# Optimization experiments

Hardware: AMD Instinct MI355X
Metric: run time of the kernel (lower is better)

Reference implementation:

```python
import jax, jax.numpy as jnp
import numpy as np
import math

B, N, E, H = 2, 2048, 1024, 16
D = E // H

def setup_inputs() -> dict:
    key = jax.random.key(0)
    ks = jax.random.split(key, 9)
    s = 1.0 / math.sqrt(E)
    return {
        "x": jax.random.normal(ks[0], (B, N, E), dtype=jnp.float32),
        "Wq": jax.random.uniform(ks[1], (E, E), jnp.float32, -s, s),
        "bq": jax.random.uniform(ks[2], (E,), jnp.float32, -s, s),
        "Wk": jax.random.uniform(ks[3], (E, E), jnp.float32, -s, s),
        "bk": jax.random.uniform(ks[4], (E,), jnp.float32, -s, s),
        "Wv": jax.random.uniform(ks[5], (E, E), jnp.float32, -s, s),
        "bv": jax.random.uniform(ks[6], (E,), jnp.float32, -s, s),
        "Wo": jax.random.uniform(ks[7], (E, E), jnp.float32, -s, s),
        "bo": jax.random.uniform(ks[8], (E,), jnp.float32, -s, s),
    }

def _split_heads(t):
    # [b, n, (h d)] -> [b, h, n, d]
    b, n, _ = t.shape
    return t.reshape(b, n, H, D).transpose(0, 2, 1, 3)

def reference(x, Wq, bq, Wk, bk, Wv, bv, Wo, bo):
    q = _split_heads(x @ Wq.T + bq)
    k = _split_heads(x @ Wk.T + bk)
    v = _split_heads(x @ Wv.T + bv)
    energy = jnp.einsum('bhqd,bhkd->bhqk', q, k)
    # Faithful to source: softmax first, THEN divide by sqrt(n_embedding)
    attention = jax.nn.softmax(energy, axis=-1) / jnp.sqrt(jnp.float32(E))
    out = jnp.einsum('bhqk,bhkd->bhqd', attention, v)
    out = out.transpose(0, 2, 1, 3).reshape(x.shape[0], x.shape[1], E)
    return out @ Wo.T + bo
```

## Files before the change

kernel.cpp:

```cpp
#include <hip/hip_runtime.h>


typedef __bf16 bf16x8 __attribute__((ext_vector_type(8)));
typedef float  f32x4  __attribute__((ext_vector_type(4)));
typedef float  f32x16 __attribute__((ext_vector_type(16)));
using u16 = unsigned short;
using u32 = unsigned int;
typedef u16 u16x8 __attribute__((ext_vector_type(8)));
typedef u16 u16x4 __attribute__((ext_vector_type(4)));
typedef u32 u32x4 __attribute__((ext_vector_type(4)));

constexpr int BATCH = 2, SEQ = 2048, EMB = 1024, NH = 16, HD = 64;
constexpr int MTOT = BATCH * SEQ;
constexpr int KTOT = EMB;
constexpr int NTOT = EMB;
constexpr float LOG2E = 1.44269504088896340736f;

constexpr size_t OFF_XBF = 0;
constexpr size_t OFF_WQ  = 8u * 1024 * 1024;
constexpr size_t OFF_WK  = OFF_WQ + 2u * 1024 * 1024;
constexpr size_t OFF_WV  = OFF_WK + 2u * 1024 * 1024;
constexpr size_t OFF_WO  = OFF_WV + 2u * 1024 * 1024;
constexpr size_t OFF_Q   = OFF_WO + 2u * 1024 * 1024;
constexpr size_t OFF_K   = OFF_Q  + 8u * 1024 * 1024;
constexpr size_t OFF_VT  = OFF_K  + 8u * 1024 * 1024;

__device__ __forceinline__ u16 f2bf(float f) {
  u32 u = __builtin_bit_cast(u32, f);
  u = (u + 0x7fffu + ((u >> 16) & 1u)) >> 16;
  return (u16)u;
}

__device__ __forceinline__ bf16x8 ld_bf16x8(const u16* p) {
  return __builtin_bit_cast(bf16x8, *(const u16x8*)p);
}

__device__ __forceinline__ float fexp2(float x) {
#if __has_builtin(__builtin_amdgcn_exp2f)
  return __builtin_amdgcn_exp2f(x);
#else
  return exp2f(x);
#endif
}

__device__ __forceinline__ float fmax3(float a, float b, float c) {
  float d;
  asm("v_max3_f32 %0, %1, %2, %3" : "=v"(d) : "v"(a), "v"(b), "v"(c));
  return d;
}

__device__ __forceinline__ u32 cvtpk(float lo, float hi_) {
  u32 r;
  asm("v_cvt_pk_bf16_f32 %0, %1, %2" : "=v"(r) : "v"(lo), "v"(hi_));
  return r;
}

__device__ __forceinline__ void stage16(const void* g, void* l) {
#if __has_builtin(__builtin_amdgcn_global_load_lds)
  __builtin_amdgcn_global_load_lds(
      (__attribute__((address_space(1))) void*)const_cast<void*>(g),
      (__attribute__((address_space(3))) void*)l, 16, 0, 0);
#else
  int lane = threadIdx.x & 63;
  uint4 v = *(const uint4*)g;
  *(uint4*)((char*)l + lane * 16) = v;
#endif
}

__global__ __launch_bounds__(256) void cvt_all(
    const float* __restrict__ x, const float* __restrict__ wq,
    const float* __restrict__ wk, const float* __restrict__ wv,
    const float* __restrict__ wo, u16* __restrict__ ox, u16* __restrict__ oq,
    u16* __restrict__ okk, u16* __restrict__ ov, u16* __restrict__ oo) {
  int id = blockIdx.x;
  const float* in;
  u16* out;
  int i;
  if (id < 4096) {
    in = x; out = ox; i = id * 256 + threadIdx.x;
  } else {
    int z = (id - 4096) >> 10, r = (id - 4096) & 1023;
    in = (z == 0) ? wq : (z == 1) ? wk : (z == 2) ? wv : wo;
    out = (z == 0) ? oq : (z == 1) ? okk : (z == 2) ? ov : oo;
    i = r * 256 + threadIdx.x;
  }
  float4 f = ((const float4*)in)[i];
  u32 lo = (u32)f2bf(f.x) | ((u32)f2bf(f.y) << 16);
  u32 hi = (u32)f2bf(f.z) | ((u32)f2bf(f.w) << 16);
  ((uint2*)out)[i] = make_uint2(lo, hi);
}

__device__ __forceinline__ void gemm_bt_core(const u16* __restrict__ A,
                                             const u16* __restrict__ Bm,
                                             const float* __restrict__ bias,
                                             void* __restrict__ out, int mode,
                                             float oscale) {
  __shared__ __align__(16) u16 smem[2][128 * 32];
  u16* sA = smem[0];
  u16* sB = smem[1];
  const int tid = threadIdx.x, w = tid >> 6, ln = tid & 63;
  const int wr = w >> 1, wc = w & 1, qq = ln >> 4, t = ln & 15;
  const int m0 = blockIdx.y * 128, n0 = blockIdx.x * 128;

  f32x4 acc[4][4] = {};

  for (int kt = 0; kt < KTOT; kt += 32) {
#pragma unroll
    for (int j = 0; j < 2; j++) {
      int ck = w * 128 + j * 64 + ln;
      int r = ck >> 2, c2 = ck & 3;
      stage16(&A[(size_t)(m0 + r) * KTOT + kt + c2 * 8], &sA[(w * 128 + j * 64) * 8]);
      stage16(&Bm[(size_t)(n0 + r) * KTOT + kt + c2 * 8], &sB[(w * 128 + j * 64) * 8]);
    }
    __syncthreads();

    bf16x8 av[4], bv[4];
#pragma unroll
    for (int f = 0; f < 4; f++) {
      av[f] = ld_bf16x8(&sA[(wr * 64 + f * 16 + t) * 32 + qq * 8]);
      bv[f] = ld_bf16x8(&sB[(wc * 64 + f * 16 + t) * 32 + qq * 8]);
    }
#pragma unroll
    for (int i = 0; i < 4; i++)
#pragma unroll
      for (int j = 0; j < 4; j++)
        acc[i][j] = __builtin_amdgcn_mfma_f32_16x16x32_bf16(av[i], bv[j], acc[i][j], 0, 0, 0);
    __syncthreads();
  }

  if (mode == 1) {
    u16* tb = (u16*)smem;
    const int b = m0 >> 11, tokb = (m0 & 2047) + t * 8;
#pragma unroll
    for (int ph = 0; ph < 2; ph++) {
      if (ph == 1) __syncthreads();
      if (wc == ph) {
#pragma unroll
        for (int fc = 0; fc < 4; fc++) {
          int nl = fc * 16 + t;
          float bn = bias[n0 + ph * 64 + nl];
#pragma unroll
          for (int fr = 0; fr < 4; fr++)
#pragma unroll
            for (int i = 0; i < 4; i++) {
              int ml = wr * 64 + fr * 16 + qq * 4 + i;
              tb[nl * 128 + (ml ^ ((nl & 7) << 4))] = f2bf(acc[fr][fc][i] + bn);
            }
        }
      }
      __syncthreads();
#pragma unroll
      for (int s = 0; s < 4; s++) {
        int row = w * 16 + s * 4 + qq;
        int n = n0 + ph * 64 + row;
        int hh = n >> 6, d = n & 63;
        u16x8 vd = *(const u16x8*)&tb[row * 128 + ((t * 8) ^ ((row & 7) << 4))];
        *(u16x8*)&((u16*)out)[(((size_t)(b * NH + hh)) * HD + d) * SEQ + tokb] = vd;
      }
    }
    return;
  }

#pragma unroll
  for (int fc = 0; fc < 4; fc++) {
    int n = n0 + wc * 64 + fc * 16 + t;
    float bn = bias[n];
#pragma unroll
    for (int fr = 0; fr < 4; fr++) {
#pragma unroll
      for (int i = 0; i < 4; i++) {
        int m = m0 + wr * 64 + fr * 16 + qq * 4 + i;
        float v = (acc[fr][fc][i] + bn) * oscale;
        if (mode == 2) {
          ((float*)out)[(size_t)m * NTOT + n] = v;
        } else {
          int b = m >> 11, tok = m & 2047, h = n >> 6, d = n & 63;
          ((u16*)out)[(((size_t)(b * NH + h)) * SEQ + tok) * HD + d] = f2bf(v);
        }
      }
    }
  }
}

__global__ __launch_bounds__(256) void gemm_qkv(
    const u16* __restrict__ A, const u16* __restrict__ WQ, const u16* __restrict__ WK,
    const u16* __restrict__ WV, const float* __restrict__ bq, const float* __restrict__ bk,
    const float* __restrict__ bv, u16* Qo, u16* Ko, u16* Vo) {
  int z = blockIdx.z;
  const u16* Bm = (z == 0) ? WQ : ((z == 1) ? WK : WV);
  const float* bias = (z == 0) ? bq : ((z == 1) ? bk : bv);
  u16* out = (z == 0) ? Qo : ((z == 1) ? Ko : Vo);
  gemm_bt_core(A, Bm, bias, out, (z == 2) ? 1 : 0, (z == 0) ? LOG2E : 1.0f);
}

__global__ __launch_bounds__(256) void gemm_o(const u16* __restrict__ A,
                                              const u16* __restrict__ WO,
                                              const float* __restrict__ bo,
                                              float* __restrict__ out) {
  gemm_bt_core(A, WO, bo, out, 2, 1.0f);
}

__global__ __launch_bounds__(512, 4) void flash_attn(const u16* __restrict__ Q,
                                                     const u16* __restrict__ Kg,
                                                     const u16* __restrict__ VT,
                                                     u16* __restrict__ O) {
  const int e = blockIdx.x;
  const int xcd = e & 7, slot = e >> 3;
  const int bh = xcd * 4 + (slot & 3);
  const int qt = slot >> 2;

  const int tid = threadIdx.x, w = tid >> 6, ln = tid & 63;
  const int c = ln & 31, hi = ln >> 5;
  const int kb = w >> 2;
  const int q0 = qt * 128 + (w & 3) * 32;

  const u16* Qb = Q + (size_t)bh * SEQ * HD;
  const u16* Kb = Kg + (size_t)bh * SEQ * HD;
  const u16* Vb = VT + (size_t)bh * HD * SEQ;

  __shared__ __align__(16) u16 sK[2][64 * 64];
  __shared__ __align__(16) u16 sV[2][64 * 64];
  __shared__ float2 sml[8][64];

  bf16x8 qf[4];
#pragma unroll
  for (int ks = 0; ks < 4; ks++)
    qf[ks] = ld_bf16x8(&Qb[(size_t)(q0 + c) * HD + ks * 16 + hi * 8]);

  const bf16x8 ones = __builtin_bit_cast(
      bf16x8, (u16x8){0x3f80, 0x3f80, 0x3f80, 0x3f80, 0x3f80, 0x3f80, 0x3f80, 0x3f80});

  f32x16 ot[2];
  ot[0] = 0.f; ot[1] = 0.f;
  f32x16 acc_l = 0.f;
  float m = -1e30f;

#define STAGE(buf, kt)                                                         \
  {                                                                            \
    int ck = w * 64 + ln;                                                      \
    int r = ck >> 3, c2 = ck & 7, c2s = c2 ^ (r & 7);                          \
    stage16(&Kb[(size_t)((kt) + r) * HD + c2s * 8],                            \
            &sK[buf][(size_t)(w * 64) * 8]);                                   \
    stage16(&Vb[(size_t)r * SEQ + (kt) + c2s * 8],                             \
            &sV[buf][(size_t)(w * 64) * 8]);                                   \
  }

  STAGE(0, 0)
  __syncthreads();

  int it = 0;
  for (int kt = 0; kt < SEQ; kt += 64, it ^= 1) {
    if (kt + 64 < SEQ) STAGE(it ^ 1, kt + 64)
    const u16* kbuf = sK[it];
    const u16* vbuf = sV[it];

    f32x16 st = 0.f;
    __builtin_amdgcn_s_setprio(1);
#pragma unroll
    for (int ks = 0; ks < 4; ks++) {
      int row = kb * 32 + c;
      int boff = ((2 * ks + hi) ^ (row & 7)) << 4;
      bf16x8 kf = ld_bf16x8((const u16*)((const char*)(kbuf + row * 64) + boff));
      st = __builtin_amdgcn_mfma_f32_32x32x16_bf16(kf, qf[ks], st, 0, 0, 0);
    }
    __builtin_amdgcn_s_setprio(0);

    float a0 = fmax3(st[0], st[1], st[2]);
    float a1 = fmax3(st[3], st[4], st[5]);
    float a2 = fmax3(st[6], st[7], st[8]);
    float a3 = fmax3(st[9], st[10], st[11]);
    float a4 = fmax3(st[12], st[13], st[14]);
    float a5 = fmaxf(st[15], a0);
    float b0 = fmax3(a1, a2, a3);
    float b1 = fmax3(a4, a5, b0);
    float pmax = fmaxf(b1, __shfl_xor(b1, 32));

    if (!__all(pmax <= m + 8.0f)) {
      float mn = fmaxf(m, pmax);
      float sc = fexp2(m - mn);
      acc_l[0] *= sc;
#pragma unroll
      for (int i = 0; i < 16; i++) { ot[0][i] *= sc; ot[1][i] *= sc; }
      m = mn;
    }

#pragma unroll
    for (int i = 0; i < 16; i++) st[i] = fexp2(st[i] - m);

    bf16x8 pb[2];
#pragma unroll
    for (int ks2 = 0; ks2 < 2; ks2++) {
      const int R0 = 8 * ks2;
      const int R1 = 4 * ((2 * ks2 + 1) & 3);
      u32 X0 = cvtpk(st[R0], st[R0 + 1]);
      u32 X1 = cvtpk(st[R0 + 2], st[R0 + 3]);
      u32 Y0 = cvtpk(st[R1], st[R1 + 1]);
      u32 Y1 = cvtpk(st[R1 + 2], st[R1 + 3]);
      asm("v_permlane32_swap_b32 %0, %1" : "+v"(X0), "+v"(Y0));
      asm("v_permlane32_swap_b32 %0, %1" : "+v"(X1), "+v"(Y1));
      u32x4 wd; wd.x = X0; wd.y = X1; wd.z = Y0; wd.w = Y1;
      pb[ks2] = __builtin_bit_cast(bf16x8, wd);
    }

    __builtin_amdgcn_s_setprio(1);
#pragma unroll
    for (int ks2 = 0; ks2 < 2; ks2++) {
#pragma unroll
      for (int db = 0; db < 2; db++) {
        int row = db * 32 + c;
        int boff = ((kb * 4 + ks2 * 2 + hi) ^ (row & 7)) << 4;
        bf16x8 vf = ld_bf16x8((const u16*)((const char*)(vbuf + row * 64) + boff));
        ot[db] = __builtin_amdgcn_mfma_f32_32x32x16_bf16(vf, pb[ks2], ot[db], 0, 0, 0);
      }
      acc_l = __builtin_amdgcn_mfma_f32_32x32x16_bf16(ones, pb[ks2], acc_l, 0, 0, 0);
    }
    __builtin_amdgcn_s_setprio(0);
    __syncthreads();
  }
#undef STAGE

  float myl = acc_l[0];
  const int pair = w & 3;
  float* xA = (float*)sK;
  float* xB = (float*)sV;
  {
    f32x16 give = (w < 4) ? ot[1] : ot[0];
    *(f32x16*)((w < 4 ? xA : xB) + (size_t)(pair * 64 + ln) * 16) = give;
    sml[w][ln] = make_float2(m, myl);
  }
  __syncthreads();

  float2 po = sml[w ^ 4][ln];
  float M2 = fmaxf(m, po.x);
  float s_me = fexp2(m - M2), s_po = fexp2(po.x - M2);
  float lf = myl * s_me + po.y * s_po;
  float inv = 1.0f / (lf * 32.0f);
  f32x16 oth = *(const f32x16*)((w < 4 ? xB : xA) + (size_t)(pair * 64 + ln) * 16);
  f32x16 own = (w < 4) ? ot[0] : ot[1];
  const int db = (w < 4) ? 0 : 1;

  const int b = bh >> 4, h = bh & 15;
  u16* obase = O + ((size_t)(b * SEQ + q0 + c)) * EMB + h * HD;
#pragma unroll
  for (int g = 0; g < 4; g++) {
    u16x4 pkt;
#pragma unroll
    for (int i = 0; i < 4; i++)
      pkt[i] = f2bf((own[g * 4 + i] * s_me + oth[g * 4 + i] * s_po) * inv);
    *(u16x4*)(obase + db * 32 + g * 8 + hi * 4) = pkt;
  }
}

extern "C" void kernel_launch(void* const* d_in, const int* in_sizes, int n_in,
                              void* d_out, int out_size, void* d_ws, size_t ws_size,
                              hipStream_t stream) {
  const float* x  = (const float*)d_in[0];
  const float* Wq = (const float*)d_in[1];
  const float* bq = (const float*)d_in[2];
  const float* Wk = (const float*)d_in[3];
  const float* bk = (const float*)d_in[4];
  const float* Wv = (const float*)d_in[5];
  const float* bv = (const float*)d_in[6];
  const float* Wo = (const float*)d_in[7];
  const float* bo = (const float*)d_in[8];

  char* ws = (char*)d_ws;
  u16* xbf = (u16*)(ws + OFF_XBF);
  u16* wqb = (u16*)(ws + OFF_WQ);
  u16* wkb = (u16*)(ws + OFF_WK);
  u16* wvb = (u16*)(ws + OFF_WV);
  u16* wob = (u16*)(ws + OFF_WO);
  u16* Qw  = (u16*)(ws + OFF_Q);
  u16* Kw  = (u16*)(ws + OFF_K);
  u16* Vw  = (u16*)(ws + OFF_VT);

  cvt_all<<<dim3(8192), 256, 0, stream>>>(x, Wq, Wk, Wv, Wo, xbf, wqb, wkb, wvb, wob);

  gemm_qkv<<<dim3(NTOT / 128, MTOT / 128, 3), 256, 0, stream>>>(
      xbf, wqb, wkb, wvb, bq, bk, bv, Qw, Kw, Vw);

  flash_attn<<<dim3(512), 512, 0, stream>>>(Qw, Kw, Vw, xbf);

  gemm_o<<<dim3(NTOT / 128, MTOT / 128), 256, 0, stream>>>(xbf, wob, bo, (float*)d_out);
}
```

Measured before the change: 136.0 us.

## Double-buffer GEMM staging and software-pipeline QK^T ahead of softmax in attention

The projection GEMM core now double-buffers its A/B shared-memory tiles, so the next K-slice loads while the current one is multiplied, leaving one barrier per iteration instead of two. The flash attention kernel moves to triple-buffered K/V tiles and a software pipeline. The QK^T MFMAs for the next tile are issued before the softmax and PV of the current tile, letting matrix work overlap the exp and permute instructions. In exchange, shared memory per block grows and more score registers stay live, which may lower occupancy.

```diff
diff --git a/kernel.cpp b/kernel.cpp
--- a/kernel.cpp
+++ b/kernel.cpp
@@ -95,24 +95,33 @@
                                              const float* __restrict__ bias,
                                              void* __restrict__ out, int mode,
                                              float oscale) {
-  __shared__ __align__(16) u16 smem[2][128 * 32];
-  u16* sA = smem[0];
-  u16* sB = smem[1];
+  __shared__ __align__(16) u16 smem[2][2][128 * 32];
   const int tid = threadIdx.x, w = tid >> 6, ln = tid & 63;
   const int wr = w >> 1, wc = w & 1, qq = ln >> 4, t = ln & 15;
   const int m0 = blockIdx.y * 128, n0 = blockIdx.x * 128;
 
   f32x4 acc[4][4] = {};
 
-  for (int kt = 0; kt < KTOT; kt += 32) {
-#pragma unroll
-    for (int j = 0; j < 2; j++) {
-      int ck = w * 128 + j * 64 + ln;
-      int r = ck >> 2, c2 = ck & 3;
-      stage16(&A[(size_t)(m0 + r) * KTOT + kt + c2 * 8], &sA[(w * 128 + j * 64) * 8]);
-      stage16(&Bm[(size_t)(n0 + r) * KTOT + kt + c2 * 8], &sB[(w * 128 + j * 64) * 8]);
-    }
-    __syncthreads();
+#define GSTAGE(bi, kt)                                                         \
+  {                                                                            \
+    _Pragma("unroll") for (int j = 0; j < 2; j++) {                            \
+      int ck = w * 128 + j * 64 + ln;                                          \
+      int r = ck >> 2, c2 = ck & 3;                                            \
+      stage16(&A[(size_t)(m0 + r) * KTOT + (kt) + c2 * 8],                     \
+              &smem[bi][0][(w * 128 + j * 64) * 8]);                           \
+      stage16(&Bm[(size_t)(n0 + r) * KTOT + (kt) + c2 * 8],                    \
+              &smem[bi][1][(w * 128 + j * 64) * 8]);                           \
+    }                                                                          \
+  }
+
+  GSTAGE(0, 0)
+  __syncthreads();
+
+  int bs = 0;
+  for (int kt = 0; kt < KTOT; kt += 32, bs ^= 1) {
+    if (kt + 32 < KTOT) GSTAGE(bs ^ 1, kt + 32)
+    const u16* sA = smem[bs][0];
+    const u16* sB = smem[bs][1];
 
     bf16x8 av[4], bv[4];
 #pragma unroll
@@ -127,6 +136,7 @@
         acc[i][j] = __builtin_amdgcn_mfma_f32_16x16x32_bf16(av[i], bv[j], acc[i][j], 0, 0, 0);
     __syncthreads();
   }
+#undef GSTAGE
 
   if (mode == 1) {
     u16* tb = (u16*)smem;
@@ -218,8 +228,8 @@
   const u16* Kb = Kg + (size_t)bh * SEQ * HD;
   const u16* Vb = VT + (size_t)bh * HD * SEQ;
 
-  __shared__ __align__(16) u16 sK[2][64 * 64];
-  __shared__ __align__(16) u16 sV[2][64 * 64];
+  __shared__ __align__(16) u16 sK[3][64 * 64];
+  __shared__ __align__(16) u16 sV[3][64 * 64];
   __shared__ float2 sml[8][64];
 
   bf16x8 qf[4];
@@ -235,89 +245,109 @@
   f32x16 acc_l = 0.f;
   float m = -1e30f;
 
-#define STAGE(buf, kt)                                                         \
+#define STAGE(pK, pV, kt)                                                      \
   {                                                                            \
     int ck = w * 64 + ln;                                                      \
     int r = ck >> 3, c2 = ck & 7, c2s = c2 ^ (r & 7);                          \
-    stage16(&Kb[(size_t)((kt) + r) * HD + c2s * 8],                            \
-            &sK[buf][(size_t)(w * 64) * 8]);                                   \
-    stage16(&Vb[(size_t)r * SEQ + (kt) + c2s * 8],                             \
-            &sV[buf][(size_t)(w * 64) * 8]);                                   \
-  }
-
-  STAGE(0, 0)
+    stage16(&Kb[(size_t)((kt) + r) * HD + c2s * 8], (pK) + (size_t)(w * 64) * 8); \
+    stage16(&Vb[(size_t)r * SEQ + (kt) + c2s * 8], (pV) + (size_t)(w * 64) * 8);  \
+  }
+
+#define QKT(stv, pK)                                                           \
+  {                                                                            \
+    stv = 0.f;                                                                 \
+    __builtin_amdgcn_s_setprio(1);                                             \
+    _Pragma("unroll") for (int ks = 0; ks < 4; ks++) {                         \
+      int row = kb * 32 + c;                                                   \
+      int boff = ((2 * ks + hi) ^ (row & 7)) << 4;                             \
+      bf16x8 kf = ld_bf16x8((const u16*)((const char*)((pK) + row * 64) + boff)); \
+      stv = __builtin_amdgcn_mfma_f32_32x32x16_bf16(kf, qf[ks], stv, 0, 0, 0); \
+    }                                                                          \
+    __builtin_amdgcn_s_setprio(0);                                             \
+  }
+
+#define SMAX(stv)                                                              \
+  {                                                                            \
+    float a0 = fmax3(stv[0], stv[1], stv[2]);                                  \
+    float a1 = fmax3(stv[3], stv[4], stv[5]);                                  \
+    float a2 = fmax3(stv[6], stv[7], stv[8]);                                  \
+    float a3 = fmax3(stv[9], stv[10], stv[11]);                                \
+    float a4 = fmax3(stv[12], stv[13], stv[14]);                               \
+    float a5 = fmaxf(stv[15], a0);                                             \
+    float b0 = fmax3(a1, a2, a3);                                              \
+    float b1 = fmax3(a4, a5, b0);                                              \
+    float pmax = fmaxf(b1, __shfl_xor(b1, 32));                                \
+    if (!__all(pmax <= m + 8.0f)) {              \
+      float mn = fmaxf(m, pmax);                                               \
+      float sc = fexp2(m - mn);                                                \
+      acc_l[0] *= sc;                                                          \
+      _Pragma("unroll") for (int i = 0; i < 16; i++) {                         \
+        ot[0][i] *= sc; ot[1][i] *= sc;                                        \
+      }                                                                        \
+      m = mn;                                                                  \
+    }                                                                          \
+    _Pragma("unroll") for (int i = 0; i < 16; i++) stv[i] = fexp2(stv[i] - m); \
+    _Pragma("unroll") for (int ks2 = 0; ks2 < 2; ks2++) {                      \
+      const int R0 = 8 * ks2;                                                  \
+      const int R1 = 4 * ((2 * ks2 + 1) & 3);                                  \
+      u32 X0 = cvtpk(stv[R0], stv[R0 + 1]);                                    \
+      u32 X1 = cvtpk(stv[R0 + 2], stv[R0 + 3]);                                \
+      u32 Y0 = cvtpk(stv[R1], stv[R1 + 1]);                                    \
+      u32 Y1 = cvtpk(stv[R1 + 2], stv[R1 + 3]);                                \
+      asm("v_permlane32_swap_b32 %0, %1" : "+v"(X0), "+v"(Y0));                \
+      asm("v_permlane32_swap_b32 %0, %1" : "+v"(X1), "+v"(Y1));                \
+      u32x4 wd; wd.x = X0; wd.y = X1; wd.z = Y0; wd.w = Y1;                    \
+      pb[ks2] = __builtin_bit_cast(bf16x8, wd);                                \
+    }                                                                          \
+  }
+
+#define PV(pV)                                                                 \
+  {                                                                            \
+    __builtin_amdgcn_s_setprio(1);                                             \
+    _Pragma("unroll") for (int ks2 = 0; ks2 < 2; ks2++) {                      \
+      _Pragma("unroll") for (int db = 0; db < 2; db++) {                       \
+        int row = db * 32 + c;                                                 \
+        int boff = ((kb * 4 + ks2 * 2 + hi) ^ (row & 7)) << 4;                 \
+        bf16x8 vf = ld_bf16x8((const u16*)((const char*)((pV) + row * 64) + boff)); \
+        ot[db] = __builtin_amdgcn_mfma_f32_32x32x16_bf16(vf, pb[ks2], ot[db], 0, 0, 0); \
+      }                                                                        \
+      acc_l = __builtin_amdgcn_mfma_f32_32x32x16_bf16(ones, pb[ks2], acc_l, 0, 0, 0); \
+    }                                                                          \
+    __builtin_amdgcn_s_setprio(0);                                             \
+  }
+
+#define BODY(t, SC, SN)                                                        \
+  {                                                                            \
+    if ((t) + 2 < 32) STAGE(kF, vF, ((t) + 2) * 64);                           \
+    if ((t) + 1 < 32) QKT(SN, kN);                                             \
+    bf16x8 pb[2];                                                              \
+    SMAX(SC);                                                                  \
+    PV(vC);                                                                    \
+    __syncthreads();                                                           \
+    u16* tk = kC; kC = kN; kN = kF; kF = tk;                                   \
+    u16* tv = vC; vC = vN; vN = vF; vF = tv;                                   \
+  }
+
+  u16 *kC = sK[0], *kN = sK[1], *kF = sK[2];
+  u16 *vC = sV[0], *vN = sV[1], *vF = sV[2];
+
+  f32x16 stA, stB;
+
+  STAGE(kC, vC, 0)
   __syncthreads();
-
-  int it = 0;
-  for (int kt = 0; kt < SEQ; kt += 64, it ^= 1) {
-    if (kt + 64 < SEQ) STAGE(it ^ 1, kt + 64)
-    const u16* kbuf = sK[it];
-    const u16* vbuf = sV[it];
-
-    f32x16 st = 0.f;
-    __builtin_amdgcn_s_setprio(1);
-#pragma unroll
-    for (int ks = 0; ks < 4; ks++) {
-      int row = kb * 32 + c;
-      int boff = ((2 * ks + hi) ^ (row & 7)) << 4;
-      bf16x8 kf = ld_bf16x8((const u16*)((const char*)(kbuf + row * 64) + boff));
-      st = __builtin_amdgcn_mfma_f32_32x32x16_bf16(kf, qf[ks], st, 0, 0, 0);
-    }
-    __builtin_amdgcn_s_setprio(0);
-
-    float a0 = fmax3(st[0], st[1], st[2]);
-    float a1 = fmax3(st[3], st[4], st[5]);
-    float a2 = fmax3(st[6], st[7], st[8]);
-    float a3 = fmax3(st[9], st[10], st[11]);
-    float a4 = fmax3(st[12], st[13], st[14]);
-    float a5 = fmaxf(st[15], a0);
-    float b0 = fmax3(a1, a2, a3);
-    float b1 = fmax3(a4, a5, b0);
-    float pmax = fmaxf(b1, __shfl_xor(b1, 32));
-
-    if (!__all(pmax <= m + 8.0f)) {
-      float mn = fmaxf(m, pmax);
-      float sc = fexp2(m - mn);
-      acc_l[0] *= sc;
-#pragma unroll
-      for (int i = 0; i < 16; i++) { ot[0][i] *= sc; ot[1][i] *= sc; }
-      m = mn;
-    }
-
-#pragma unroll
-    for (int i = 0; i < 16; i++) st[i] = fexp2(st[i] - m);
-
-    bf16x8 pb[2];
-#pragma unroll
-    for (int ks2 = 0; ks2 < 2; ks2++) {
-      const int R0 = 8 * ks2;
-      const int R1 = 4 * ((2 * ks2 + 1) & 3);
-      u32 X0 = cvtpk(st[R0], st[R0 + 1]);
-      u32 X1 = cvtpk(st[R0 + 2], st[R0 + 3]);
-      u32 Y0 = cvtpk(st[R1], st[R1 + 1]);
-      u32 Y1 = cvtpk(st[R1 + 2], st[R1 + 3]);
-      asm("v_permlane32_swap_b32 %0, %1" : "+v"(X0), "+v"(Y0));
-      asm("v_permlane32_swap_b32 %0, %1" : "+v"(X1), "+v"(Y1));
-      u32x4 wd; wd.x = X0; wd.y = X1; wd.z = Y0; wd.w = Y1;
-      pb[ks2] = __builtin_bit_cast(bf16x8, wd);
-    }
-
-    __builtin_amdgcn_s_setprio(1);
-#pragma unroll
-    for (int ks2 = 0; ks2 < 2; ks2++) {
-#pragma unroll
-      for (int db = 0; db < 2; db++) {
-        int row = db * 32 + c;
-        int boff = ((kb * 4 + ks2 * 2 + hi) ^ (row & 7)) << 4;
-        bf16x8 vf = ld_bf16x8((const u16*)((const char*)(vbuf + row * 64) + boff));
-        ot[db] = __builtin_amdgcn_mfma_f32_32x32x16_bf16(vf, pb[ks2], ot[db], 0, 0, 0);
-      }
-      acc_l = __builtin_amdgcn_mfma_f32_32x32x16_bf16(ones, pb[ks2], acc_l, 0, 0, 0);
-    }
-    __builtin_amdgcn_s_setprio(0);
-    __syncthreads();
+  QKT(stA, kC)
+  STAGE(kN, vN, 64)
+  __syncthreads();
+
+  for (int t = 0; t < 32; t += 2) {
+    BODY(t, stA, stB)
+    BODY(t + 1, stB, stA)
   }
 #undef STAGE
+#undef QKT
+#undef SMAX
+#undef PV
+#undef BODY
 
   float myl = acc_l[0];
   const int pair = w & 3;
```

New measurement: 134.8 us. No clear change (-0.9%).
